# Kernel optimization log

Hardware: AMD Instinct MI355X
Metric: run time of the kernel (lower is better)

## Reference

```python
import jax, jax.numpy as jnp
import numpy as np
from jax import lax

B, H, W = 32, 40, 256
FREQ = 40            # freq_num
WIND = 0.5           # wind_size (seconds)
KF = 5               # input_filter_kernel (odd -> 'same' length)
CNN_OUT = 64 * 36 * 252  # out_channels[-1] * (H-4) * (W-4)


def setup_inputs() -> dict:
    key = jax.random.key(0)
    ks = jax.random.split(key, 9)
    return {
        "inputs": jax.random.normal(ks[0], (B, 1, H, W), jnp.float32),
        "w0": jax.random.normal(ks[1], (32, 1, 3, 3), jnp.float32) * 0.1,
        "b0": jax.random.normal(ks[2], (32,), jnp.float32) * 0.05,
        "w1": jax.random.normal(ks[3], (64, 32, 3, 3), jnp.float32) * 0.05,
        "b1": jax.random.normal(ks[4], (64,), jnp.float32) * 0.05,
        "wf": jax.random.normal(ks[5], (1, 1, 1, KF), jnp.float32) * 0.2,
        "bf": jax.random.normal(ks[6], (1,), jnp.float32) * 0.05,
        "wr": jax.random.normal(ks[7], (FREQ, CNN_OUT), jnp.float32) * 1e-3,
        "br": jax.random.normal(ks[8], (FREQ,), jnp.float32) * 0.05,
    }


def _conv2d(x, w, padding):
    return lax.conv_general_dilated(
        x, w, window_strides=(1, 1), padding=padding,
        dimension_numbers=("NCHW", "OIHW", "NCHW"))


def reference(inputs, w0, b0, w1, b1, wf, bf, wr, br):
    b, _, h, w_len = inputs.shape
    # input_filter: Conv1d(1,1,KF, padding=KF//2) applied independently per
    # frequency row -> equivalent to a 2D conv with a (1,KF) kernel.
    p = KF // 2
    feats = _conv2d(inputs, wf, [(0, 0), (p, p)]) + bf[None, :, None, None]  # [B,1,H,W]

    # conv stack with ReLU
    x = jax.nn.relu(_conv2d(inputs, w0, "VALID") + b0[None, :, None, None])
    x = jax.nn.relu(_conv2d(x, w1, "VALID") + b1[None, :, None, None])

    gates = jax.nn.sigmoid(x.reshape(b, -1) @ wr.T + br)

    fs = (1.0 / WIND) * jnp.linspace(1.0, FREQ, FREQ)          # [FREQ]
    wtd_mean_mod = jnp.mean(gates * fs[None, :])               # scalar

    # Fused modulation transform: instead of the per-frequency python loop
    # with materialized [B,H,W] broadcasts, compute sin/cos bases [FREQ,W]
    # and reduce over time with a single einsum each.
    t = jnp.linspace(0.0, WIND, w_len)                          # [W]
    phase = (2.0 * np.pi) * fs[:, None] * t[None, :]            # [FREQ,W]
    f0 = feats[:, 0]                                            # [B,H,W]
    inv_w = jnp.float32(1.0 / w_len)
    sins = jnp.einsum("fw,bhw->bfh", jnp.sin(phase), f0) * inv_w  # mean over W
    coss = jnp.einsum("fw,bhw->bfh", jnp.cos(phase), f0) * inv_w
    mag = jnp.sqrt(sins * sins + coss * coss)                   # [B,FREQ,H]
    mods = (mag * gates[:, :, None]).reshape(b, FREQ * h)       # cat over freq, dim=1
    return mods, wtd_mean_mod
```

## Files before the change

kernel.cpp:

```cpp
#include <hip/hip_runtime.h>
#include <hip/hip_bf16.h>
#include <math.h>

#define BB   32
#define HH   40
#define WW   256
#define NF   40
#define H1N  36
#define W1N  252
#define KCNN 580608
#define KPW  96

typedef __attribute__((ext_vector_type(8))) short bf16x8;
typedef __attribute__((ext_vector_type(4))) float f32x4;

static __device__ __forceinline__ unsigned short f2bf(float v) {
    __hip_bfloat16 h = __float2bfloat16(v);
    return *(unsigned short*)&h;
}

static __device__ __forceinline__ bf16x8 packbf(float4 lo, float4 hi) {
    bf16x8 r;
    r[0] = (short)f2bf(lo.x); r[1] = (short)f2bf(lo.y);
    r[2] = (short)f2bf(lo.z); r[3] = (short)f2bf(lo.w);
    r[4] = (short)f2bf(hi.x); r[5] = (short)f2bf(hi.y);
    r[6] = (short)f2bf(hi.z); r[7] = (short)f2bf(hi.w);
    return r;
}

__global__ void k0_prep(const float* __restrict__ w1, unsigned short* __restrict__ w1c,
                        float* __restrict__ gacc8, float* __restrict__ sintab,
                        float* __restrict__ costab, float* __restrict__ out) {
    int o = blockIdx.x * 256 + threadIdx.x;
    int c0  = o & 31;
    int c1  = (o >> 5) & 63;
    int tap = o >> 11;
    w1c[o] = f2bf(w1[(c1 * 32 + c0) * 9 + tap]);
    if (o < 10240) {
        int f = o >> 8, w = o & 255;
        float ph = 6.283185307179586f * (float)(f + 1) * (1.0f / 255.0f) * (float)w;
        sintab[o] = sinf(ph);
        costab[o] = cosf(ph);
        gacc8[o] = 0.0f;
    }
    if (o == 0) out[51200] = 0.0f;
}

__global__ __launch_bounds__(256) void k1_conv(
        const float* __restrict__ inp, const float* __restrict__ w0,
        const float* __restrict__ b0, const unsigned short* __restrict__ w1c,
        const float* __restrict__ b1, unsigned short* __restrict__ xbf) {
    __shared__ __align__(16) char smem[33856];
    float* ins = (float*)smem;
    unsigned short* y0T = (unsigned short*)(smem + 2176);
    unsigned short* stg = (unsigned short*)smem;

    const int jt = blockIdx.x;
    const int it = blockIdx.y;
    const int b  = blockIdx.z;
    const int i0 = it * 4;
    const int j0 = jt * 64;
    const int tid = threadIdx.x;

    if (tid < 136) {
        int r  = tid / 17, c4 = tid - r * 17;
        float4 v = {0.f, 0.f, 0.f, 0.f};
        if (jt < 3 || c4 < 16)
            v = *(const float4*)(inp + (b * HH + i0 + r) * WW + j0 + c4 * 4);
        *(float4*)(ins + r * 68 + c4 * 4) = v;
    }
    __syncthreads();

    {
        const int c0 = tid & 31;
        const int pg = tid >> 5;
        if (pg < 6) {
            float wreg[9];
            #pragma unroll
            for (int k = 0; k < 9; ++k) wreg[k] = w0[c0 * 9 + k];
            const float bias = b0[c0];
            const float4* rp0 = (const float4*)(ins + (pg    ) * 68);
            const float4* rp1 = (const float4*)(ins + (pg + 1) * 68);
            const float4* rp2 = (const float4*)(ins + (pg + 2) * 68);
            unsigned short* yrow = y0T + pg * 66 * 40 + c0;
            float4 a0 = rp0[0], a1 = rp1[0], a2 = rp2[0];
            #pragma unroll 2
            for (int ch = 0; ch < 8; ++ch) {
                float4 b0v = rp0[2 * ch + 1], c0v = rp0[2 * ch + 2];
                float4 b1v = rp1[2 * ch + 1], c1v = rp1[2 * ch + 2];
                float4 b2v = rp2[2 * ch + 1], c2v = rp2[2 * ch + 2];
                float r0[12] = {a0.x,a0.y,a0.z,a0.w,b0v.x,b0v.y,b0v.z,b0v.w,c0v.x,c0v.y,c0v.z,c0v.w};
                float r1[12] = {a1.x,a1.y,a1.z,a1.w,b1v.x,b1v.y,b1v.z,b1v.w,c1v.x,c1v.y,c1v.z,c1v.w};
                float r2[12] = {a2.x,a2.y,a2.z,a2.w,b2v.x,b2v.y,b2v.z,b2v.w,c2v.x,c2v.y,c2v.z,c2v.w};
                #pragma unroll
                for (int t = 0; t < 8; ++t) {
                    int col = ch * 8 + t;
                    float a = bias;
                    #pragma unroll
                    for (int kj = 0; kj < 3; ++kj) {
                        a = fmaf(r0[t + kj], wreg[kj],     a);
                        a = fmaf(r1[t + kj], wreg[3 + kj], a);
                        a = fmaf(r2[t + kj], wreg[6 + kj], a);
                    }
                    float v = (j0 + col < 254) ? fmaxf(a, 0.0f) : 0.0f;
                    yrow[col * 40] = f2bf(v);
                }
                a0 = c0v; a1 = c1v; a2 = c2v;
            }
            {
                float t0[4] = {a0.x, a0.y, a0.z, a0.w};
                float t1[4] = {a1.x, a1.y, a1.z, a1.w};
                float t2[4] = {a2.x, a2.y, a2.z, a2.w};
                #pragma unroll
                for (int t = 0; t < 2; ++t) {
                    int col = 64 + t;
                    float a = bias;
                    #pragma unroll
                    for (int kj = 0; kj < 3; ++kj) {
                        a = fmaf(t0[t + kj], wreg[kj],     a);
                        a = fmaf(t1[t + kj], wreg[3 + kj], a);
                        a = fmaf(t2[t + kj], wreg[6 + kj], a);
                    }
                    float v = (j0 + col < 254) ? fmaxf(a, 0.0f) : 0.0f;
                    yrow[col * 40] = f2bf(v);
                }
            }
        }
    }
    __syncthreads();

    const int w    = tid >> 6;
    const int lane = tid & 63;
    const int l15  = lane & 15;
    const int quad = lane >> 4;

    float biasr[4][4];
    #pragma unroll
    for (int mt = 0; mt < 4; ++mt)
        #pragma unroll
        for (int rg = 0; rg < 4; ++rg)
            biasr[mt][rg] = b1[mt * 16 + quad * 4 + rg];

    f32x4 acc[4][4];
    #pragma unroll
    for (int mt = 0; mt < 4; ++mt)
        #pragma unroll
        for (int nt = 0; nt < 4; ++nt)
            acc[mt][nt] = (f32x4){0.f, 0.f, 0.f, 0.f};

    #pragma unroll
    for (int ki = 0; ki < 3; ++ki) {
        #pragma unroll
        for (int kj = 0; kj < 3; ++kj) {
            const int tap = ki * 3 + kj;
            bf16x8 af[4], bfr[4];
            #pragma unroll
            for (int mt = 0; mt < 4; ++mt)
                af[mt] = *(const bf16x8*)(w1c + ((tap * 64 + mt * 16 + l15) * 32 + quad * 8));
            #pragma unroll
            for (int nt = 0; nt < 4; ++nt)
                bfr[nt] = *(const bf16x8*)(y0T + (((w + ki) * 66 + nt * 16 + l15 + kj) * 40 + quad * 8));
            #pragma unroll
            for (int mt = 0; mt < 4; ++mt)
                #pragma unroll
                for (int nt = 0; nt < 4; ++nt)
                    acc[mt][nt] = __builtin_amdgcn_mfma_f32_16x16x32_bf16(
                        af[mt], bfr[nt], acc[mt][nt], 0, 0, 0);
        }
    }

    __syncthreads();
    #pragma unroll
    for (int mt = 0; mt < 4; ++mt)
        #pragma unroll
        for (int nt = 0; nt < 4; ++nt)
            #pragma unroll
            for (int rg = 0; rg < 4; ++rg) {
                int c1 = mt * 16 + quad * 4 + rg;
                int j  = nt * 16 + l15;
                int jr = (j + (((c1 >> 2) & 3) << 4)) & 63;
                float v = fmaxf(acc[mt][nt][rg] + biasr[mt][rg], 0.0f);
                stg[(c1 * 4 + w) * 64 + jr] = f2bf(v);
            }
    __syncthreads();

    const int limit = (j0 + 64 <= W1N) ? 64 : (W1N - j0);
    for (int it2 = 0; it2 < 16; ++it2) {
        int cc = it2 * 256 + tid;
        int e  = cc * 4;
        int c1 = e >> 8;
        int w2 = (e >> 6) & 3;
        int jb = e & 63;
        if (jb < limit) {
            int jr = (jb + (((c1 >> 2) & 3) << 4)) & 63;
            *(uint2*)(xbf + (size_t)b * KCNN + (c1 * H1N + i0 + w2) * W1N + j0 + jb) =
                *(const uint2*)(stg + (c1 * 4 + w2) * 64 + jr);
        }
    }
}

__global__ __launch_bounds__(256) void k2_gemm(
        const unsigned short* __restrict__ xbf, const float* __restrict__ wr,
        float* __restrict__ gacc8) {
    __shared__ float red[4][32][41];

    const int tid  = threadIdx.x;
    const int wv   = tid >> 6;
    const int lane = tid & 63;
    const int l15  = lane & 15;
    const int quad = lane >> 4;
    const size_t kw = (size_t)(blockIdx.x * 4 + wv) * KPW;

    const unsigned short* ap0 = xbf + (size_t)l15 * KCNN + kw + quad * 8;
    const unsigned short* ap1 = ap0 + (size_t)16 * KCNN;
    const float* bp0 = wr + (size_t)l15 * KCNN + kw + quad * 8;
    const float* bp1 = bp0 + (size_t)16 * KCNN;
    const bool v2 = (l15 < 8);
    const float* bp2 = bp0 + (size_t)32 * KCNN;

    f32x4 acc[2][3];
    #pragma unroll
    for (int mt = 0; mt < 2; ++mt)
        #pragma unroll
        for (int nt = 0; nt < 3; ++nt)
            acc[mt][nt] = (f32x4){0.f, 0.f, 0.f, 0.f};

    const float4 fz = {0.f, 0.f, 0.f, 0.f};
    bf16x8 a0c, a1c, a0n, a1n;
    float4 bw[3][2], bwn[3][2];

    a0c = *(const bf16x8*)ap0;
    a1c = *(const bf16x8*)ap1;
    bw[0][0] = *(const float4*)bp0; bw[0][1] = *(const float4*)(bp0 + 4);
    bw[1][0] = *(const float4*)bp1; bw[1][1] = *(const float4*)(bp1 + 4);
    if (v2) { bw[2][0] = *(const float4*)bp2; bw[2][1] = *(const float4*)(bp2 + 4); }
    else    { bw[2][0] = fz; bw[2][1] = fz; }

    for (int c = 0; c < 3; ++c) {
        if (c < 2) {
            const int o2 = (c + 1) * 32;
            a0n = *(const bf16x8*)(ap0 + o2);
            a1n = *(const bf16x8*)(ap1 + o2);
            bwn[0][0] = *(const float4*)(bp0 + o2); bwn[0][1] = *(const float4*)(bp0 + o2 + 4);
            bwn[1][0] = *(const float4*)(bp1 + o2); bwn[1][1] = *(const float4*)(bp1 + o2 + 4);
            if (v2) { bwn[2][0] = *(const float4*)(bp2 + o2); bwn[2][1] = *(const float4*)(bp2 + o2 + 4); }
            else    { bwn[2][0] = fz; bwn[2][1] = fz; }
        }
        #pragma unroll
        for (int nt = 0; nt < 3; ++nt) {
            bf16x8 bfrag = packbf(bw[nt][0], bw[nt][1]);
            acc[0][nt] = __builtin_amdgcn_mfma_f32_16x16x32_bf16(a0c, bfrag, acc[0][nt], 0, 0, 0);
            acc[1][nt] = __builtin_amdgcn_mfma_f32_16x16x32_bf16(a1c, bfrag, acc[1][nt], 0, 0, 0);
        }
        if (c < 2) {
            a0c = a0n; a1c = a1n;
            #pragma unroll
            for (int nt = 0; nt < 3; ++nt) { bw[nt][0] = bwn[nt][0]; bw[nt][1] = bwn[nt][1]; }
        }
    }

    #pragma unroll
    for (int mt = 0; mt < 2; ++mt)
        #pragma unroll
        for (int nt = 0; nt < 3; ++nt)
            #pragma unroll
            for (int rg = 0; rg < 4; ++rg) {
                int bb = mt * 16 + quad * 4 + rg;
                int ff = nt * 16 + l15;
                if (ff < NF) red[wv][bb][ff] = acc[mt][nt][rg];
            }
    __syncthreads();
    float* myg = gacc8 + (size_t)(blockIdx.x & 7) * 1280;
    for (int p = tid; p < 1280; p += 256) {
        int bb = p / 40, ff = p - bb * 40;
        float s = 0.0f;
        #pragma unroll
        for (int w = 0; w < 4; ++w) s += red[w][bb][ff];
        atomicAdd(myg + p, s);
    }
}

__global__ __launch_bounds__(320) void k4_mods(
        const float* __restrict__ inp, const float* __restrict__ sintab,
        const float* __restrict__ costab, const float* __restrict__ wf,
        const float* __restrict__ bfp, const float* __restrict__ gacc8,
        const float* __restrict__ br, float* __restrict__ out) {
    const int f = blockIdx.x, b = blockIdx.y;
    const int tid = threadIdx.x;
    const int h  = tid >> 3;
    const int wl = tid & 7;

    float s = 0.0f;
    #pragma unroll
    for (int r = 0; r < 8; ++r) s += gacc8[r * 1280 + b * 40 + f];
    const float g = 1.0f / (1.0f + __expf(-(s + br[f])));
    if (tid == 0)
        atomicAdd(out + 51200, g * (2.0f * (float)(f + 1)) * (1.0f / 1280.0f));

    float wfv[5];
    #pragma unroll
    for (int t = 0; t < 5; ++t) wfv[t] = wf[t];
    const float bias = bfp[0];
    const float* row  = inp + (b * HH + h) * WW;
    const float* srow = sintab + f * 256;
    const float* crow = costab + f * 256;
    float sa = 0.0f, ca = 0.0f;
    for (int m = 0; m < 32; ++m) {
        int w = wl + 8 * m;
        float feat = bias;
        #pragma unroll
        for (int d = -2; d <= 2; ++d) {
            int wc = w + d;
            if (wc >= 0 && wc < WW) feat = fmaf(row[wc], wfv[d + 2], feat);
        }
        sa = fmaf(srow[w], feat, sa);
        ca = fmaf(crow[w], feat, ca);
    }
    #pragma unroll
    for (int off = 4; off >= 1; off >>= 1) {
        sa += __shfl_xor(sa, off, 8);
        ca += __shfl_xor(ca, off, 8);
    }
    if (wl == 0) {
        float mag = sqrtf(sa * sa + ca * ca) * (1.0f / 256.0f);
        out[b * 1600 + f * 40 + h] = mag * g;
    }
}

extern "C" void kernel_launch(void* const* d_in, const int* in_sizes, int n_in,
                              void* d_out, int out_size, void* d_ws, size_t ws_size,
                              hipStream_t stream) {
    const float* inp = (const float*)d_in[0];
    const float* w0  = (const float*)d_in[1];
    const float* b0  = (const float*)d_in[2];
    const float* w1  = (const float*)d_in[3];
    const float* b1  = (const float*)d_in[4];
    const float* wf  = (const float*)d_in[5];
    const float* bf_ = (const float*)d_in[6];
    const float* wr  = (const float*)d_in[7];
    const float* br  = (const float*)d_in[8];
    float* out = (float*)d_out;

    char* ws = (char*)d_ws;
    unsigned short* xbf = (unsigned short*)ws;
    unsigned short* w1c = (unsigned short*)(ws + 37158912);
    float* gacc8  = (float*)(ws + 37195776);
    float* sintab = (float*)(ws + 37236736);
    float* costab = (float*)(ws + 37277696);

    k0_prep<<<72, 256, 0, stream>>>(w1, w1c, gacc8, sintab, costab, out);
    k1_conv<<<dim3(4, 9, 32), 256, 0, stream>>>(inp, w0, b0, w1c, b1, xbf);
    k2_gemm<<<1512, 256, 0, stream>>>(xbf, wr, gacc8);
    k4_mods<<<dim3(40, 32), 320, 0, stream>>>(inp, sintab, costab, wf, bf_, gacc8, br, out);
}
```

Measured before the change: 228.7 us.

## Stage GEMM operand tiles through LDS with coalesced loads and once-only bf16 conversion

```diff
diff --git a/kernel.cpp b/kernel.cpp
--- a/kernel.cpp
+++ b/kernel.cpp
@@ -9,7 +9,8 @@
 #define H1N  36
 #define W1N  252
 #define KCNN 580608
-#define KPW  96
+#define KT   256
+#define NBLK2 1134
 
 typedef __attribute__((ext_vector_type(8))) short bf16x8;
 typedef __attribute__((ext_vector_type(4))) float f32x4;
@@ -17,15 +18,6 @@
 static __device__ __forceinline__ unsigned short f2bf(float v) {
     __hip_bfloat16 h = __float2bfloat16(v);
     return *(unsigned short*)&h;
-}
-
-static __device__ __forceinline__ bf16x8 packbf(float4 lo, float4 hi) {
-    bf16x8 r;
-    r[0] = (short)f2bf(lo.x); r[1] = (short)f2bf(lo.y);
-    r[2] = (short)f2bf(lo.z); r[3] = (short)f2bf(lo.w);
-    r[4] = (short)f2bf(hi.x); r[5] = (short)f2bf(hi.y);
-    r[6] = (short)f2bf(hi.z); r[7] = (short)f2bf(hi.w);
-    return r;
 }
 
 __global__ void k0_prep(const float* __restrict__ w1, unsigned short* __restrict__ w1c,
@@ -202,21 +194,21 @@
 __global__ __launch_bounds__(256) void k2_gemm(
         const unsigned short* __restrict__ xbf, const float* __restrict__ wr,
         float* __restrict__ gacc8) {
-    __shared__ float red[4][32][41];
+    __shared__ __align__(16) char smem[42240];
+    unsigned short* lx = (unsigned short*)smem;
+    unsigned short* lw = (unsigned short*)(smem + 16896);
+    float (*red)[32][41] = (float (*)[32][41])smem;
 
     const int tid  = threadIdx.x;
     const int wv   = tid >> 6;
     const int lane = tid & 63;
     const int l15  = lane & 15;
     const int quad = lane >> 4;
-    const size_t kw = (size_t)(blockIdx.x * 4 + wv) * KPW;
-
-    const unsigned short* ap0 = xbf + (size_t)l15 * KCNN + kw + quad * 8;
-    const unsigned short* ap1 = ap0 + (size_t)16 * KCNN;
-    const float* bp0 = wr + (size_t)l15 * KCNN + kw + quad * 8;
-    const float* bp1 = bp0 + (size_t)16 * KCNN;
-    const bool v2 = (l15 < 8);
-    const float* bp2 = bp0 + (size_t)32 * KCNN;
+
+    for (int i = tid; i < 264; i += 256) {
+        int row = 40 + i / 33, seg = i % 33;
+        *(bf16x8*)(lw + row * 264 + seg * 8) = (bf16x8){0,0,0,0,0,0,0,0};
+    }
 
     f32x4 acc[2][3];
     #pragma unroll
@@ -225,40 +217,41 @@
         for (int nt = 0; nt < 3; ++nt)
             acc[mt][nt] = (f32x4){0.f, 0.f, 0.f, 0.f};
 
-    const float4 fz = {0.f, 0.f, 0.f, 0.f};
-    bf16x8 a0c, a1c, a0n, a1n;
-    float4 bw[3][2], bwn[3][2];
-
-    a0c = *(const bf16x8*)ap0;
-    a1c = *(const bf16x8*)ap1;
-    bw[0][0] = *(const float4*)bp0; bw[0][1] = *(const float4*)(bp0 + 4);
-    bw[1][0] = *(const float4*)bp1; bw[1][1] = *(const float4*)(bp1 + 4);
-    if (v2) { bw[2][0] = *(const float4*)bp2; bw[2][1] = *(const float4*)(bp2 + 4); }
-    else    { bw[2][0] = fz; bw[2][1] = fz; }
-
-    for (int c = 0; c < 3; ++c) {
-        if (c < 2) {
-            const int o2 = (c + 1) * 32;
-            a0n = *(const bf16x8*)(ap0 + o2);
-            a1n = *(const bf16x8*)(ap1 + o2);
-            bwn[0][0] = *(const float4*)(bp0 + o2); bwn[0][1] = *(const float4*)(bp0 + o2 + 4);
-            bwn[1][0] = *(const float4*)(bp1 + o2); bwn[1][1] = *(const float4*)(bp1 + o2 + 4);
-            if (v2) { bwn[2][0] = *(const float4*)(bp2 + o2); bwn[2][1] = *(const float4*)(bp2 + o2 + 4); }
-            else    { bwn[2][0] = fz; bwn[2][1] = fz; }
-        }
-        #pragma unroll
-        for (int nt = 0; nt < 3; ++nt) {
-            bf16x8 bfrag = packbf(bw[nt][0], bw[nt][1]);
-            acc[0][nt] = __builtin_amdgcn_mfma_f32_16x16x32_bf16(a0c, bfrag, acc[0][nt], 0, 0, 0);
-            acc[1][nt] = __builtin_amdgcn_mfma_f32_16x16x32_bf16(a1c, bfrag, acc[1][nt], 0, 0, 0);
-        }
-        if (c < 2) {
-            a0c = a0n; a1c = a1n;
-            #pragma unroll
-            for (int nt = 0; nt < 3; ++nt) { bw[nt][0] = bwn[nt][0]; bw[nt][1] = bwn[nt][1]; }
-        }
-    }
-
+    for (int it = 0; it < 2; ++it) {
+        const size_t kt = (size_t)(blockIdx.x + it * NBLK2) * KT;
+        __syncthreads();
+
+        for (int i = tid; i < 1024; i += 256) {
+            int row = i >> 5, seg = i & 31;
+            *(bf16x8*)(lx + row * 264 + seg * 8) =
+                *(const bf16x8*)(xbf + (size_t)row * KCNN + kt + seg * 8);
+        }
+        for (int i = tid; i < 2560; i += 256) {
+            int row = i >> 6, seg = i & 63;
+            float4 v = *(const float4*)(wr + (size_t)row * KCNN + kt + seg * 4);
+            ushort4 p = { f2bf(v.x), f2bf(v.y), f2bf(v.z), f2bf(v.w) };
+            *(ushort4*)(lw + row * 264 + seg * 4) = p;
+        }
+        __syncthreads();
+
+        #pragma unroll
+        for (int c = 0; c < 2; ++c) {
+            const int lk = wv * 64 + c * 32;
+            bf16x8 af[2], bfr[3];
+            af[0] = *(const bf16x8*)(lx + (l15     ) * 264 + lk + quad * 8);
+            af[1] = *(const bf16x8*)(lx + (16 + l15) * 264 + lk + quad * 8);
+            #pragma unroll
+            for (int nt = 0; nt < 3; ++nt)
+                bfr[nt] = *(const bf16x8*)(lw + (nt * 16 + l15) * 264 + lk + quad * 8);
+            #pragma unroll
+            for (int nt = 0; nt < 3; ++nt) {
+                acc[0][nt] = __builtin_amdgcn_mfma_f32_16x16x32_bf16(af[0], bfr[nt], acc[0][nt], 0, 0, 0);
+                acc[1][nt] = __builtin_amdgcn_mfma_f32_16x16x32_bf16(af[1], bfr[nt], acc[1][nt], 0, 0, 0);
+            }
+        }
+    }
+
+    __syncthreads();
     #pragma unroll
     for (int mt = 0; mt < 2; ++mt)
         #pragma unroll
@@ -350,6 +343,6 @@
 
     k0_prep<<<72, 256, 0, stream>>>(w1, w1c, gacc8, sintab, costab, out);
     k1_conv<<<dim3(4, 9, 32), 256, 0, stream>>>(inp, w0, b0, w1c, b1, xbf);
-    k2_gemm<<<1512, 256, 0, stream>>>(xbf, wr, gacc8);
+    k2_gemm<<<NBLK2, 256, 0, stream>>>(xbf, wr, gacc8);
     k4_mods<<<dim3(40, 32), 320, 0, stream>>>(inp, sintab, costab, wf, bf_, gacc8, br, out);
 }
```

After: 240.9 us. 1.05x slower.
